# Performance work log

Hardware: AMD Instinct MI355X
Metric: run time of the kernel (lower is better)

## Reference

```python
import jax, jax.numpy as jnp
import numpy as np

EMBED_DIM = 2048
NUM_HEADS = 16
HEAD_DIM = EMBED_DIM // NUM_HEADS  # 128
EPS = 1e-12  # F.normalize default eps


def setup_inputs() -> dict:
    key = jax.random.key(0)
    k1, k2, k3 = jax.random.split(key, 3)
    x = jax.random.normal(k1, (4, 2048, EMBED_DIM), dtype=jnp.float32)
    # nn.Linear(embed_dim, 3*embed_dim): weight [3E, E], bias [3E]
    W = jax.random.normal(k2, (3 * EMBED_DIM, EMBED_DIM), dtype=jnp.float32) * (EMBED_DIM ** -0.5)
    b = jax.random.normal(k3, (3 * EMBED_DIM,), dtype=jnp.float32) * 0.02
    return {"x": x, "W": W, "b": b}


def _l2_normalize(t):
    # matches F.normalize(p=2, dim=-1): t / max(||t||, eps)
    n = jnp.sqrt(jnp.sum(t * t, axis=-1, keepdims=True))
    return t / jnp.maximum(n, EPS)


def reference(x, W, b):
    B, L, E = x.shape
    H, HD = NUM_HEADS, HEAD_DIM
    y = x @ W.T + b  # [B, L, 3E]
    # rearrange '... l (h c) -> ... h l c' with c = 3*HD, then chunk into q,k,v
    y = y.reshape(B, L, H, 3, HD)
    q = jnp.transpose(y[..., 0, :], (0, 2, 1, 3))  # [B, H, L, HD]
    k = jnp.transpose(y[..., 1, :], (0, 2, 1, 3))
    v = jnp.transpose(y[..., 2, :], (0, 2, 1, 3))
    q = _l2_normalize(q)
    k = _l2_normalize(k)
    # cosine attention, scale=1, non-causal, no mask
    scores = jnp.einsum('bhld,bhmd->bhlm', q, k)
    attn = jax.nn.softmax(scores, axis=-1)
    out = jnp.einsum('bhlm,bhmd->bhld', attn, v)  # [B, H, L, HD]
    return jnp.transpose(out, (0, 2, 1, 3)).reshape(B, L, E)
```

## Files before the change

kernel.cpp:

```cpp
#include <hip/hip_runtime.h>
#include <hip/hip_bf16.h>

typedef __bf16 bf16_t;
typedef __bf16 bf16x8 __attribute__((ext_vector_type(8)));
typedef __bf16 bf16x4 __attribute__((ext_vector_type(4)));
typedef __bf16 bf16x2 __attribute__((ext_vector_type(2)));
typedef float f32x4 __attribute__((ext_vector_type(4)));

#define MFMA16(a,b,c) __builtin_amdgcn_mfma_f32_16x16x32_bf16((a),(b),(c),0,0,0)
#define AS3(p) ((__attribute__((address_space(3))) void*)(p))
#define AS1(p) ((const __attribute__((address_space(1))) void*)(p))

constexpr int B_ = 4, L_ = 2048, E_ = 2048, H_ = 16, HD_ = 128;
constexpr size_t QK_ELEMS = (size_t)B_ * H_ * L_ * HD_;
constexpr size_t NX = (size_t)B_ * L_ * E_;
constexpr size_t NW = (size_t)3 * E_ * E_;

__global__ __launch_bounds__(256) void cvt(
    const float* __restrict__ X, const float* __restrict__ W, bf16_t* __restrict__ dst)
{
  size_t e = ((size_t)blockIdx.x * 256 + threadIdx.x) * 4;
  f32x4 v = (e < NX) ? *(const f32x4*)&X[e] : *(const f32x4*)&W[e - NX];
  bf16x4 o;
  for (int u = 0; u < 4; ++u) o[u] = (__bf16)v[u];
  *(bf16x4*)&dst[e] = o;
}

constexpr int BM = 256, BN = 256, BK = 64, KTILES = E_ / BK;

__global__ __launch_bounds__(512, 2) void gemm_qkv(
    const bf16_t* __restrict__ Xb, const bf16_t* __restrict__ Wb, const float* __restrict__ bias,
    bf16_t* __restrict__ q, bf16_t* __restrict__ k, bf16_t* __restrict__ vT)
{
  __shared__ alignas(16) bf16_t Al[2][BM * BK];
  __shared__ alignas(16) bf16_t Bl[2][BN * BK];
  const int tid = threadIdx.x;
  const int wave = tid >> 6, lane = tid & 63;
  const int wm = wave >> 2, wn = wave & 3;

  const int bid = blockIdx.y * 24 + blockIdx.x;
  const int swz = (bid & 7) * 96 + (bid >> 3);
  const int bx = swz % 24, by = swz / 24;
  const int m0 = by * BM, n0 = bx * BN;

  const int r8 = lane >> 3;
  const int cSrc = (lane & 7) ^ r8;
  const bf16_t* gA = &Xb[(size_t)(m0 + wave * 8 + r8) * E_ + cSrc * 8];
  const bf16_t* gB = &Wb[(size_t)(n0 + wave * 8 + r8) * E_ + cSrc * 8];

#define STAGE(buf, t) do { \
    const bf16_t* sa_ = gA + (t) * BK; \
    const bf16_t* sb_ = gB + (t) * BK; \
    bf16_t* la_ = &Al[buf][wave * 512]; \
    bf16_t* lb_ = &Bl[buf][wave * 512]; \
    __builtin_amdgcn_global_load_lds(AS1(sa_),                       AS3(la_),         16, 0, 0); \
    __builtin_amdgcn_global_load_lds(AS1(sa_ + (size_t)64 * E_),     AS3(la_ +  4096), 16, 0, 0); \
    __builtin_amdgcn_global_load_lds(AS1(sa_ + (size_t)128 * E_),    AS3(la_ +  8192), 16, 0, 0); \
    __builtin_amdgcn_global_load_lds(AS1(sa_ + (size_t)192 * E_),    AS3(la_ + 12288), 16, 0, 0); \
    __builtin_amdgcn_global_load_lds(AS1(sb_),                       AS3(lb_),         16, 0, 0); \
    __builtin_amdgcn_global_load_lds(AS1(sb_ + (size_t)64 * E_),     AS3(lb_ +  4096), 16, 0, 0); \
    __builtin_amdgcn_global_load_lds(AS1(sb_ + (size_t)128 * E_),    AS3(lb_ +  8192), 16, 0, 0); \
    __builtin_amdgcn_global_load_lds(AS1(sb_ + (size_t)192 * E_),    AS3(lb_ + 12288), 16, 0, 0); \
  } while (0)

  const int rowf = lane & 15, q4 = lane >> 4, rkey = lane & 7;
#define RD_A(buf, mtg, ks) (*(const bf16x8*)&Al[buf][(wm * 128 + (mtg) * 16 + rowf) * 64 + ((((ks) << 2) | q4) ^ rkey) * 8])
#define RD_B(buf, nt, ks)  (*(const bf16x8*)&Bl[buf][(wn * 64  + (nt) * 16 + rowf) * 64 + ((((ks) << 2) | q4) ^ rkey) * 8])
#define SBAR() __builtin_amdgcn_s_barrier()

  const f32x4 fzero = {0.f, 0.f, 0.f, 0.f};
  f32x4 acc[8][4];
#pragma unroll
  for (int i = 0; i < 8; ++i)
#pragma unroll
    for (int j = 0; j < 4; ++j) acc[i][j] = fzero;

  STAGE(0, 0);
  STAGE(1, 1);
  asm volatile("s_waitcnt vmcnt(8)" ::: "memory");
  SBAR();

  for (int t = 0; t < KTILES; ++t) {
    const int cur = t & 1;
    bf16x8 bfr[4][2];
#pragma unroll
    for (int p = 0; p < 4; ++p) {
      bf16x8 af[2][2];
#pragma unroll
      for (int i = 0; i < 2; ++i)
#pragma unroll
        for (int ks = 0; ks < 2; ++ks)
          af[i][ks] = RD_A(cur, p * 2 + i, ks);
      if (p == 0) {
#pragma unroll
        for (int nt = 0; nt < 4; ++nt)
#pragma unroll
          for (int ks = 0; ks < 2; ++ks)
            bfr[nt][ks] = RD_B(cur, nt, ks);
      }
      SBAR();
      __builtin_amdgcn_s_setprio(1);
#pragma unroll
      for (int i = 0; i < 2; ++i)
#pragma unroll
        for (int nt = 0; nt < 4; ++nt)
#pragma unroll
          for (int ks = 0; ks < 2; ++ks)
            acc[p * 2 + i][nt] = MFMA16(af[i][ks], bfr[nt][ks], acc[p * 2 + i][nt]);
      __builtin_amdgcn_s_setprio(0);
      if (p < 3) SBAR();
    }
    asm volatile("s_waitcnt lgkmcnt(0)" ::: "memory");
    SBAR();
    if (t + 2 < KTILES) {
      STAGE(cur, t + 2);
      asm volatile("s_waitcnt vmcnt(8)" ::: "memory");
    } else {
      asm volatile("s_waitcnt vmcnt(0)" ::: "memory");
    }
    SBAR();
  }
#undef STAGE
#undef RD_A
#undef RD_B

  __syncthreads();

  const int b  = m0 >> 11;
  const int l0 = m0 & (L_ - 1);
  const int gch = 2 * bx + (wn >> 1);
  const int h   = gch / 3;
  const int which = gch % 3;
  const int rlane = (lane >> 4) << 2;
  const int clane = lane & 15;

  float bcol[4];
#pragma unroll
  for (int nt = 0; nt < 4; ++nt)
    bcol[nt] = bias[n0 + wn * 64 + nt * 16 + clane];
#pragma unroll
  for (int mt = 0; mt < 8; ++mt)
#pragma unroll
    for (int nt = 0; nt < 4; ++nt)
#pragma unroll
      for (int r = 0; r < 4; ++r)
        acc[mt][nt][r] += bcol[nt];

  float* NormS = (float*)&Al[0][0];
  if (which < 2) {
#pragma unroll
    for (int mt = 0; mt < 8; ++mt)
#pragma unroll
      for (int r = 0; r < 4; ++r) {
        float sq = 0.f;
#pragma unroll
        for (int nt = 0; nt < 4; ++nt) sq += acc[mt][nt][r] * acc[mt][nt][r];
#pragma unroll
        for (int off = 8; off; off >>= 1) sq += __shfl_xor(sq, off);
        if (clane == 0) {
          int row = wm * 128 + mt * 16 + rlane + r;
          NormS[((wn >> 1) * 256 + row) * 2 + (wn & 1)] = sq;
        }
      }
  }
  __syncthreads();

  if (which < 2) {
    bf16_t* base = ((which == 0) ? q : k) + ((size_t)(b * H_ + h) * L_) * HD_;
#pragma unroll
    for (int mt = 0; mt < 8; ++mt)
#pragma unroll
      for (int r = 0; r < 4; ++r) {
        int row = wm * 128 + mt * 16 + rlane + r;
        float tot = NormS[((wn >> 1) * 256 + row) * 2] + NormS[((wn >> 1) * 256 + row) * 2 + 1];
        float invn = 1.0f / fmaxf(sqrtf(tot), 1e-12f);
        bf16_t* rowp = base + (size_t)(l0 + row) * HD_;
#pragma unroll
        for (int nt = 0; nt < 4; ++nt) {
          int hd = (wn & 1) * 64 + nt * 16 + clane;
          rowp[hd] = (__bf16)(acc[mt][nt][r] * invn);
        }
      }
  } else {
    bf16_t* base = vT + ((size_t)(b * H_ + h) * HD_) * L_;
#pragma unroll
    for (int mt = 0; mt < 8; ++mt)
#pragma unroll
      for (int r = 0; r < 4; ++r) {
        int l = l0 + wm * 128 + mt * 16 + rlane + r;
#pragma unroll
        for (int nt = 0; nt < 4; ++nt) {
          int hd = (wn & 1) * 64 + nt * 16 + clane;
          base[(size_t)hd * L_ + l] = (__bf16)acc[mt][nt][r];
        }
      }
  }
}

__device__ __forceinline__ int swz128(int r, int c) {
  return r * 128 + ((((c >> 3) ^ (r & 15)) & 15) << 3) + (c & 7);
}
__device__ __forceinline__ int swz64(int r, int c) {
  return r * 64 + ((((c >> 3) ^ (r & 7)) & 7) << 3) + (c & 7);
}

__global__ __launch_bounds__(256) void attn(
    const bf16_t* __restrict__ q, const bf16_t* __restrict__ k,
    const bf16_t* __restrict__ vT, float* __restrict__ out)
{
  __shared__ alignas(16) bf16_t Ks[64 * 128];
  __shared__ alignas(16) bf16_t Vts[128 * 64];
  __shared__ alignas(16) bf16_t Ps[128 * 64];

  const int tid = threadIdx.x, wave = tid >> 6, lane = tid & 63;
  const int bh = blockIdx.y;
  const int q0 = blockIdx.x * 128;
  const int rowf = lane & 15, kq8 = (lane >> 4) * 8;

  const bf16_t* qbase = q + ((size_t)bh * L_ + q0) * HD_;
  const bf16_t* kbh = k + (size_t)bh * L_ * HD_;
  const bf16_t* vbh = vT + (size_t)bh * HD_ * L_;

  bf16x8 qf[4][2];
  for (int kk4 = 0; kk4 < 4; ++kk4)
    for (int mt = 0; mt < 2; ++mt)
      qf[kk4][mt] = *(const bf16x8*)&qbase[(size_t)(wave * 32 + mt * 16 + rowf) * HD_ + kk4 * 32 + kq8];

  const f32x4 fzero = {0.f, 0.f, 0.f, 0.f};
  f32x4 o[2][8];
  for (int mt = 0; mt < 2; ++mt)
    for (int nt = 0; nt < 8; ++nt) o[mt][nt] = fzero;
  float lrow[2][4];
  for (int mt = 0; mt < 2; ++mt)
    for (int r = 0; r < 4; ++r) lrow[mt][r] = 0.f;

  bf16x8 kreg[4], vreg[4];

  for (int i = 0; i < 4; ++i) {
    int e = (i * 256 + tid) * 8;
    kreg[i] = *(const bf16x8*)&kbh[e];
  }
  for (int i = 0; i < 4; ++i) {
    int e = (i * 256 + tid) * 8;
    int d = e >> 6, c = e & 63;
    vreg[i] = *(const bf16x8*)&vbh[(size_t)d * L_ + c];
  }
  for (int i = 0; i < 4; ++i) {
    int e = (i * 256 + tid) * 8;
    *(bf16x8*)&Ks[swz128(e >> 7, e & 127)] = kreg[i];
  }
  for (int i = 0; i < 4; ++i) {
    int e = (i * 256 + tid) * 8;
    int d = e >> 6, c = e & 63;
    *(bf16x8*)&Vts[swz64(d, c)] = vreg[i];
  }
  __syncthreads();

  for (int j0 = 0; j0 < L_; j0 += 64) {
    const bool more = (j0 + 64 < L_);
    if (more) {
      const int jn = j0 + 64;
      for (int i = 0; i < 4; ++i) {
        int e = (i * 256 + tid) * 8;
        kreg[i] = *(const bf16x8*)&kbh[(size_t)jn * HD_ + e];
      }
      for (int i = 0; i < 4; ++i) {
        int e = (i * 256 + tid) * 8;
        int d = e >> 6, c = e & 63;
        vreg[i] = *(const bf16x8*)&vbh[(size_t)d * L_ + jn + c];
      }
    }

    f32x4 s[2][4];
    for (int mt = 0; mt < 2; ++mt)
      for (int nt = 0; nt < 4; ++nt) s[mt][nt] = fzero;
    __builtin_amdgcn_s_setprio(1);
    for (int kk = 0; kk < 128; kk += 32) {
      bf16x8 bk4[4];
      for (int nt = 0; nt < 4; ++nt) bk4[nt] = *(const bf16x8*)&Ks[swz128(nt * 16 + rowf, kk + kq8)];
      for (int mt = 0; mt < 2; ++mt)
        for (int nt = 0; nt < 4; ++nt)
          s[mt][nt] = MFMA16(qf[kk >> 5][mt], bk4[nt], s[mt][nt]);
    }
    __builtin_amdgcn_s_setprio(0);

    for (int mt = 0; mt < 2; ++mt)
      for (int nt = 0; nt < 4; ++nt)
        for (int r = 0; r < 4; ++r) {
          float p = __expf(s[mt][nt][r]);
          lrow[mt][r] += p;
          int rr = wave * 32 + mt * 16 + ((lane >> 4) << 2) + r;
          int cc = nt * 16 + (lane & 15);
          Ps[swz64(rr, cc)] = (__bf16)p;
        }

    __builtin_amdgcn_s_setprio(1);
    for (int kk = 0; kk < 64; kk += 32) {
      bf16x8 ap[2];
      for (int mt = 0; mt < 2; ++mt)
        ap[mt] = *(const bf16x8*)&Ps[swz64(wave * 32 + mt * 16 + rowf, kk + kq8)];
      for (int nt = 0; nt < 8; ++nt) {
        bf16x8 bvv = *(const bf16x8*)&Vts[swz64(nt * 16 + rowf, kk + kq8)];
        for (int mt = 0; mt < 2; ++mt)
          o[mt][nt] = MFMA16(ap[mt], bvv, o[mt][nt]);
      }
    }
    __builtin_amdgcn_s_setprio(0);

    __syncthreads();
    if (more) {
      for (int i = 0; i < 4; ++i) {
        int e = (i * 256 + tid) * 8;
        *(bf16x8*)&Ks[swz128(e >> 7, e & 127)] = kreg[i];
      }
      for (int i = 0; i < 4; ++i) {
        int e = (i * 256 + tid) * 8;
        int d = e >> 6, c = e & 63;
        *(bf16x8*)&Vts[swz64(d, c)] = vreg[i];
      }
      __syncthreads();
    }
  }

  const int b = bh >> 4, h = bh & 15;
  for (int mt = 0; mt < 2; ++mt) {
    for (int r = 0; r < 4; ++r) {
      float lsum = lrow[mt][r];
      for (int off = 8; off; off >>= 1) lsum += __shfl_xor(lsum, off);
      float inv = 1.0f / lsum;
      int l = q0 + wave * 32 + mt * 16 + ((lane >> 4) << 2) + r;
      float* op = out + (((size_t)b * L_ + l) * H_ + h) * HD_;
      for (int nt = 0; nt < 8; ++nt) {
        int d = nt * 16 + (lane & 15);
        op[d] = o[mt][nt][r] * inv;
      }
    }
  }
}

extern "C" void kernel_launch(void* const* d_in, const int* in_sizes, int n_in,
                              void* d_out, int out_size, void* d_ws, size_t ws_size,
                              hipStream_t stream)
{
  const float* X    = (const float*)d_in[0];
  const float* W    = (const float*)d_in[1];
  const float* bias = (const float*)d_in[2];
  float* out = (float*)d_out;

  bf16_t* Xb = (bf16_t*)d_out;
  bf16_t* Wb = Xb + NX;

  bf16_t* q  = (bf16_t*)d_ws;
  bf16_t* k  = q + QK_ELEMS;
  bf16_t* vT = k + QK_ELEMS;

  cvt<<<dim3((NX + NW) / (256 * 4)), 256, 0, stream>>>(X, W, Xb);
  gemm_qkv<<<dim3(24, 32), 512, 0, stream>>>(Xb, Wb, bias, q, k, vT);
  attn<<<dim3(16, 64), 256, 0, stream>>>(q, k, vT, out);
}
```

Measured before the change: 637.0 us.

## Double-buffer K/V tiles via direct global-to-LDS loads and remap blocks for locality

Replaces the register-staged K/V prefetch with global_load_lds async copies into double-buffered shared memory. The source addresses are pre-swizzled so the existing swizzled reads stay valid. This removes one barrier per iteration and frees the registers that held the staged tiles. It also remaps the block index so that consecutive blocks spread across heads, which changes cache and L2 locality. The cost is twice the K/V LDS footprint, which may lower occupancy, and reliance on the async copies finishing before the single barrier.

```diff
diff --git a/kernel.cpp b/kernel.cpp
--- a/kernel.cpp
+++ b/kernel.cpp
@@ -208,18 +208,37 @@
     const bf16_t* __restrict__ q, const bf16_t* __restrict__ k,
     const bf16_t* __restrict__ vT, float* __restrict__ out)
 {
-  __shared__ alignas(16) bf16_t Ks[64 * 128];
-  __shared__ alignas(16) bf16_t Vts[128 * 64];
+  __shared__ alignas(16) bf16_t Ks[2][64 * 128];
+  __shared__ alignas(16) bf16_t Vts[2][128 * 64];
   __shared__ alignas(16) bf16_t Ps[128 * 64];
 
   const int tid = threadIdx.x, wave = tid >> 6, lane = tid & 63;
-  const int bh = blockIdx.y;
-  const int q0 = blockIdx.x * 128;
+
+  const int sid = blockIdx.y * 16 + blockIdx.x;
+  const int vid = (sid & 7) * 128 + (sid >> 3);
+  const int bh = vid >> 4;
+  const int q0 = (vid & 15) << 7;
+
   const int rowf = lane & 15, kq8 = (lane >> 4) * 8;
 
   const bf16_t* qbase = q + ((size_t)bh * L_ + q0) * HD_;
   const bf16_t* kbh = k + (size_t)bh * L_ * HD_;
   const bf16_t* vbh = vT + (size_t)bh * HD_ * L_;
+
+#define STAGE_KV(buf, j0v) do { \
+    for (int i_ = 0; i_ < 4; ++i_) { \
+      int r_ = i_ * 16 + wave * 4 + (lane >> 4); \
+      int c_ = (lane & 15) ^ (r_ & 15); \
+      __builtin_amdgcn_global_load_lds(AS1(kbh + (size_t)((j0v) + r_) * HD_ + c_ * 8), \
+                                       AS3(&Ks[buf][i_ * 2048 + wave * 512]), 16, 0, 0); \
+    } \
+    for (int i_ = 0; i_ < 4; ++i_) { \
+      int d_ = i_ * 32 + wave * 8 + (lane >> 3); \
+      int c_ = (lane & 7) ^ (d_ & 7); \
+      __builtin_amdgcn_global_load_lds(AS1(vbh + (size_t)d_ * L_ + (j0v) + c_ * 8), \
+                                       AS3(&Vts[buf][i_ * 2048 + wave * 512]), 16, 0, 0); \
+    } \
+  } while (0)
 
   bf16x8 qf[4][2];
   for (int kk4 = 0; kk4 < 4; ++kk4)
@@ -234,42 +253,12 @@
   for (int mt = 0; mt < 2; ++mt)
     for (int r = 0; r < 4; ++r) lrow[mt][r] = 0.f;
 
-  bf16x8 kreg[4], vreg[4];
-
-  for (int i = 0; i < 4; ++i) {
-    int e = (i * 256 + tid) * 8;
-    kreg[i] = *(const bf16x8*)&kbh[e];
-  }
-  for (int i = 0; i < 4; ++i) {
-    int e = (i * 256 + tid) * 8;
-    int d = e >> 6, c = e & 63;
-    vreg[i] = *(const bf16x8*)&vbh[(size_t)d * L_ + c];
-  }
-  for (int i = 0; i < 4; ++i) {
-    int e = (i * 256 + tid) * 8;
-    *(bf16x8*)&Ks[swz128(e >> 7, e & 127)] = kreg[i];
-  }
-  for (int i = 0; i < 4; ++i) {
-    int e = (i * 256 + tid) * 8;
-    int d = e >> 6, c = e & 63;
-    *(bf16x8*)&Vts[swz64(d, c)] = vreg[i];
-  }
+  STAGE_KV(0, 0);
   __syncthreads();
+  int cur = 0;
 
   for (int j0 = 0; j0 < L_; j0 += 64) {
-    const bool more = (j0 + 64 < L_);
-    if (more) {
-      const int jn = j0 + 64;
-      for (int i = 0; i < 4; ++i) {
-        int e = (i * 256 + tid) * 8;
-        kreg[i] = *(const bf16x8*)&kbh[(size_t)jn * HD_ + e];
-      }
-      for (int i = 0; i < 4; ++i) {
-        int e = (i * 256 + tid) * 8;
-        int d = e >> 6, c = e & 63;
-        vreg[i] = *(const bf16x8*)&vbh[(size_t)d * L_ + jn + c];
-      }
-    }
+    if (j0 + 64 < L_) STAGE_KV(cur ^ 1, j0 + 64);
 
     f32x4 s[2][4];
     for (int mt = 0; mt < 2; ++mt)
@@ -277,7 +266,7 @@
     __builtin_amdgcn_s_setprio(1);
     for (int kk = 0; kk < 128; kk += 32) {
       bf16x8 bk4[4];
-      for (int nt = 0; nt < 4; ++nt) bk4[nt] = *(const bf16x8*)&Ks[swz128(nt * 16 + rowf, kk + kq8)];
+      for (int nt = 0; nt < 4; ++nt) bk4[nt] = *(const bf16x8*)&Ks[cur][swz128(nt * 16 + rowf, kk + kq8)];
       for (int mt = 0; mt < 2; ++mt)
         for (int nt = 0; nt < 4; ++nt)
           s[mt][nt] = MFMA16(qf[kk >> 5][mt], bk4[nt], s[mt][nt]);
@@ -300,7 +289,7 @@
       for (int mt = 0; mt < 2; ++mt)
         ap[mt] = *(const bf16x8*)&Ps[swz64(wave * 32 + mt * 16 + rowf, kk + kq8)];
       for (int nt = 0; nt < 8; ++nt) {
-        bf16x8 bvv = *(const bf16x8*)&Vts[swz64(nt * 16 + rowf, kk + kq8)];
+        bf16x8 bvv = *(const bf16x8*)&Vts[cur][swz64(nt * 16 + rowf, kk + kq8)];
         for (int mt = 0; mt < 2; ++mt)
           o[mt][nt] = MFMA16(ap[mt], bvv, o[mt][nt]);
       }
@@ -308,19 +297,9 @@
     __builtin_amdgcn_s_setprio(0);
 
     __syncthreads();
-    if (more) {
-      for (int i = 0; i < 4; ++i) {
-        int e = (i * 256 + tid) * 8;
-        *(bf16x8*)&Ks[swz128(e >> 7, e & 127)] = kreg[i];
-      }
-      for (int i = 0; i < 4; ++i) {
-        int e = (i * 256 + tid) * 8;
-        int d = e >> 6, c = e & 63;
-        *(bf16x8*)&Vts[swz64(d, c)] = vreg[i];
-      }
-      __syncthreads();
-    }
-  }
+    cur ^= 1;
+  }
+#undef STAGE_KV
 
   const int b = bh >> 4, h = bh & 15;
   for (int mt = 0; mt < 2; ++mt) {
```

Measured after the change: 635.6 us. No clear change (-0.2%).
